# Optimization experiments

Hardware: AMD Instinct MI355X
Metric: run time of the kernel (lower is better)

## Reference

```python
import jax, jax.numpy as jnp
import numpy as np

B, N, C_IN = 32, 1024, 128
F0, F1, F2 = 64, 64, 64
OUT = 10
RATIOS = (0.8, 0.8)
EPS = 1e-5


def setup_inputs() -> dict:
    key = jax.random.key(0)
    ks = jax.random.split(key, 16)
    N_nodes = jax.random.randint(ks[0], (B,), N // 2, N + 1)
    mask = (jnp.arange(N)[None, :] < N_nodes[:, None]).astype(jnp.float32)
    x = jax.random.normal(ks[1], (B, N, C_IN), dtype=jnp.float32)
    # sparse-ish symmetric binary adjacency restricted to valid nodes
    A = (jax.random.uniform(ks[2], (B, N, N)) < 0.02).astype(jnp.float32)
    A = jnp.maximum(A, jnp.swapaxes(A, 1, 2))
    A = A * mask[:, :, None] * mask[:, None, :]
    def lin(k, fi, fo):
        b = 1.0 / np.sqrt(fi)
        kw, kb = jax.random.split(k)
        return (jax.random.uniform(kw, (fi, fo), minval=-b, maxval=b),
                jax.random.uniform(kb, (fo,), minval=-b, maxval=b))
    W0, b0 = lin(ks[3], C_IN, F0)
    W1, b1 = lin(ks[4], F0, F1)
    W2, b2 = lin(ks[5], F1, F2)
    bp0 = 1.0 / np.sqrt(F0)
    p0 = jax.random.uniform(ks[6], (F0, 1), minval=-bp0, maxval=bp0)
    bp1 = 1.0 / np.sqrt(F1)
    p1 = jax.random.uniform(ks[7], (F1, 1), minval=-bp1, maxval=bp1)
    Wfc, bfc = lin(ks[8], F2, OUT)
    return {"x": x, "A": A, "mask": mask, "N_nodes": N_nodes,
            "W0": W0, "b0": b0, "W1": W1, "b1": b1, "W2": W2, "b2": b2,
            "p0": p0, "p1": p1, "Wfc": Wfc, "bfc": bfc}


def _gconv(x, A, W, b):
    # Kipf-Welling normalized Laplacian conv, batched dense
    n = A.shape[1]
    A_hat = A + jnp.eye(n, dtype=A.dtype)[None]
    D = (jnp.sum(A_hat, axis=1) + EPS) ** -0.5  # [B,N]
    L = D[:, :, None] * A_hat * D[:, None, :]
    h = jnp.einsum('bnm,bmc->bnc', L, x) @ W + b
    return jax.nn.relu(h)


def _pool(x, A, mask, N_nodes, p, ratio):
    Bc, Nc, C = x.shape
    y = (x.reshape(Bc * Nc, C) @ p).reshape(Bc, Nc)
    y = y / jnp.sqrt(jnp.sum(p ** 2))
    N_remove = (N_nodes.astype(jnp.float32) * (1.0 - ratio)).astype(N_nodes.dtype)
    # remove the N_remove lowest-scoring valid nodes per graph
    y_eff = jnp.where(mask > 0, y, jnp.inf)
    ranks = jnp.argsort(jnp.argsort(y_eff, axis=1), axis=1)  # ascending rank
    new_mask = mask * (ranks >= N_remove[:, None]).astype(mask.dtype)
    x = x * jnp.tanh(y)[:, :, None] * new_mask[:, :, None]
    A = new_mask[:, :, None] * A * new_mask[:, None, :]
    return x, A, new_mask, N_nodes - N_remove


def reference(x, A, mask, N_nodes, W0, b0, W1, b1, W2, b2, p0, p1, Wfc, bfc):
    x = _gconv(x, A, W0, b0)
    x, A, mask, N_nodes = _pool(x, A, mask, N_nodes, p0, RATIOS[0])
    x = _gconv(x, A, W1, b1)
    x, A, mask, N_nodes = _pool(x, A, mask, N_nodes, p1, RATIOS[1])
    x = _gconv(x, A, W2, b2)
    x = jnp.max(x, axis=1)  # global max pool over nodes [B,F2]
    return x @ Wfc + bfc
```

## Files before the change

kernel.cpp:

```cpp
#include <hip/hip_runtime.h>
#include <cstdint>
#include <cstddef>

#define BB 32
#define NN 1024
#define CIN 128
#define FF 64
#define NOUT 10
#define CAP 128
#define EPSV 1e-5f

__global__ __launch_bounds__(256) void k_front(const float* __restrict__ A,
                                               const float* __restrict__ x,
                                               const float* __restrict__ W0,
                                               const int* __restrict__ Nn,
                                               const float* __restrict__ b2f,
                                               float* __restrict__ gmax,
                                               unsigned short* __restrict__ adj,
                                               int* __restrict__ cnt,
                                               float* __restrict__ c1,
                                               float* __restrict__ c2,
                                               float* __restrict__ T) {
    __shared__ __align__(16) float Wl[64 * 64];
    int tid = threadIdx.x;
    int wave = tid >> 6, lane = tid & 63;
    if (blockIdx.x >= 10240) {
        for (int i = tid; i < BB * 64; i += 256)
            gmax[i] = fmaxf(b2f[i & 63], 0.f);
        return;
    }
    if (blockIdx.x >= 8192) {
        int gid = blockIdx.x - 8192;
        int b = gid & 31;
        int cch = gid >> 5;
        if (cch * 16 >= Nn[b]) return;
        int row0 = (b << 10) + cch * 16;
        int rsub = lane >> 4, f0 = (lane & 15) * 4;
        int r = row0 + wave * 4 + rsub;
        const float4* xr = (const float4*)(x + (size_t)r * CIN);
        float4 acc = {0.f, 0.f, 0.f, 0.f};
#pragma unroll
        for (int kc = 0; kc < 2; ++kc) {
            if (kc) __syncthreads();
            for (int t = tid; t < 64 * 16; t += 256)
                ((float4*)Wl)[t] = ((const float4*)W0)[kc * 1024 + t];
            __syncthreads();
#pragma unroll 4
            for (int k4 = 0; k4 < 16; ++k4) {
                float4 xv = xr[kc * 16 + k4];
                float4 w0 = *(const float4*)&Wl[(k4 * 4 + 0) * 64 + f0];
                float4 w1 = *(const float4*)&Wl[(k4 * 4 + 1) * 64 + f0];
                float4 w2 = *(const float4*)&Wl[(k4 * 4 + 2) * 64 + f0];
                float4 w3 = *(const float4*)&Wl[(k4 * 4 + 3) * 64 + f0];
                acc.x += xv.x * w0.x; acc.y += xv.x * w0.y; acc.z += xv.x * w0.z; acc.w += xv.x * w0.w;
                acc.x += xv.y * w1.x; acc.y += xv.y * w1.y; acc.z += xv.y * w1.z; acc.w += xv.y * w1.w;
                acc.x += xv.z * w2.x; acc.y += xv.z * w2.y; acc.z += xv.z * w2.z; acc.w += xv.z * w2.w;
                acc.x += xv.w * w3.x; acc.y += xv.w * w3.y; acc.z += xv.w * w3.z; acc.w += xv.w * w3.w;
            }
        }
        *(float4*)&T[(size_t)r * 64 + f0] = acc;
    } else {
        int r = blockIdx.x * 4 + wave;
        int b = r >> 10;
        int Nb = Nn[b];
        int rl = r & 1023;
        if (rl >= Nb) {
            if (lane == 0) {
                cnt[r] = 0;
                float D = 1.0f / sqrtf(1.0f + EPSV);
                c1[r] = D;
                c2[r] = D * D;
            }
            return;
        }
        unsigned short* adjs = ((unsigned short*)Wl) + wave * CAP;
        const float4* Arow = (const float4*)(A + (size_t)r * NN);
        int nch = (Nb + 255) >> 8;
        float4 z4 = {0.f, 0.f, 0.f, 0.f};
        float4 v0 = Arow[lane];
        float4 v1 = Arow[64 + lane];
        float4 v2 = (nch > 2) ? Arow[128 + lane] : z4;
        float4 v3 = (nch > 3) ? Arow[192 + lane] : z4;
        int c = 0;
        unsigned long long lt = (lane == 0) ? 0ULL : ((1ULL << lane) - 1ULL);
        float4 vv[4] = {v0, v1, v2, v3};
#pragma unroll
        for (int it = 0; it < 4; ++it) {
            float4 v = vv[it];
            int j0 = it * 256 + lane * 4;
            unsigned long long m0 = __ballot(v.x != 0.f);
            unsigned long long m1 = __ballot(v.y != 0.f);
            unsigned long long m2 = __ballot(v.z != 0.f);
            unsigned long long m3 = __ballot(v.w != 0.f);
            int before = __popcll(m0 & lt) + __popcll(m1 & lt) +
                         __popcll(m2 & lt) + __popcll(m3 & lt);
            int p = c + before;
            if (v.x != 0.f) { if (p < CAP) adjs[p] = (unsigned short)(j0 + 0); ++p; }
            if (v.y != 0.f) { if (p < CAP) adjs[p] = (unsigned short)(j0 + 1); ++p; }
            if (v.z != 0.f) { if (p < CAP) adjs[p] = (unsigned short)(j0 + 2); ++p; }
            if (v.w != 0.f) { if (p < CAP) adjs[p] = (unsigned short)(j0 + 3); ++p; }
            c += __popcll(m0) + __popcll(m1) + __popcll(m2) + __popcll(m3);
        }
        int cc = (c > CAP) ? CAP : c;
        uint32_t* dst = (uint32_t*)(adj + (size_t)r * CAP);
        if (lane * 2 < cc) dst[lane] = ((const uint32_t*)adjs)[lane];
        if (lane == 0) {
            cnt[r] = cc;
            float D = 1.0f / sqrtf((float)c + 1.0f + EPSV);
            c1[r] = D;
            c2[r] = D * D;
        }
    }
}

__global__ __launch_bounds__(256) void k_mid(const unsigned short* __restrict__ adj,
                                             const int* __restrict__ cnt,
                                             const float* __restrict__ nm,
                                             float* __restrict__ c1, float* __restrict__ c2,
                                             const float* __restrict__ Xin,
                                             const float* __restrict__ W,
                                             const float* __restrict__ y,
                                             float* __restrict__ T,
                                             const int* __restrict__ Nn) {
    __shared__ __align__(16) float Wl[64 * 64];
    int tid = threadIdx.x;
    if (blockIdx.x >= 8192) {
        int gid = blockIdx.x - 8192;
        int b = gid & 31;
        int cch = gid >> 5;
        if (cch * 16 >= Nn[b]) return;
        int row0 = (b << 10) + cch * 16;
        for (int t = tid; t < 64 * 16; t += 256)
            ((float4*)Wl)[t] = ((const float4*)W)[t];
        __syncthreads();
        int wave = tid >> 6, lane = tid & 63;
        int rsub = lane >> 4, f0 = (lane & 15) * 4;
        int r = row0 + wave * 4 + rsub;
        float sc = tanhf(y[r]) * nm[r];
        const float4* xr = (const float4*)(Xin + (size_t)r * 64);
        float4 acc = {0.f, 0.f, 0.f, 0.f};
#pragma unroll 4
        for (int k4 = 0; k4 < 16; ++k4) {
            float4 xv = xr[k4];
            float4 w0 = *(const float4*)&Wl[(k4 * 4 + 0) * 64 + f0];
            float4 w1 = *(const float4*)&Wl[(k4 * 4 + 1) * 64 + f0];
            float4 w2 = *(const float4*)&Wl[(k4 * 4 + 2) * 64 + f0];
            float4 w3 = *(const float4*)&Wl[(k4 * 4 + 3) * 64 + f0];
            acc.x += xv.x * w0.x; acc.y += xv.x * w0.y; acc.z += xv.x * w0.z; acc.w += xv.x * w0.w;
            acc.x += xv.y * w1.x; acc.y += xv.y * w1.y; acc.z += xv.y * w1.z; acc.w += xv.y * w1.w;
            acc.x += xv.z * w2.x; acc.y += xv.z * w2.y; acc.z += xv.z * w2.z; acc.w += xv.z * w2.w;
            acc.x += xv.w * w3.x; acc.y += xv.w * w3.y; acc.z += xv.w * w3.z; acc.w += xv.w * w3.w;
        }
        acc.x *= sc; acc.y *= sc; acc.z *= sc; acc.w *= sc;
        *(float4*)&T[(size_t)r * 64 + f0] = acc;
    } else {
        int wave = tid >> 6, lane = tid & 63;
        int r = blockIdx.x * 4 + wave;
        int b = r >> 10;
        if ((r & 1023) >= Nn[b]) return;
        const unsigned short* arow = adj + (size_t)r * CAP;
        const float* nmb = nm + (b << 10);
        int n = cnt[r];
        float s = 0.f;
        if (lane < n)      s  = nmb[arow[lane]];
        if (lane + 64 < n) s += nmb[arow[lane + 64]];
        for (int sh = 32; sh; sh >>= 1) s += __shfl_xor(s, sh, 64);
        if (lane == 0) {
            float m = nm[r];
            float D = 1.0f / sqrtf(m * s + 1.0f + EPSV);
            c1[r] = m * D;
            c2[r] = D * D;
        }
    }
}

__global__ __launch_bounds__(256) void k_spmm(const unsigned short* __restrict__ adj,
                                              const int* __restrict__ cnt,
                                              const float* __restrict__ c1,
                                              const float* __restrict__ c2,
                                              const float* __restrict__ T,
                                              const float* __restrict__ bias,
                                              float* __restrict__ X,
                                              const float* __restrict__ p,
                                              float* __restrict__ y,
                                              float* __restrict__ gmax,
                                              const int* __restrict__ Nn) {
    __shared__ __align__(16) float c1s[NN];
    __shared__ float red[4][64];
    int b   = blockIdx.x & 31;
    int cch = blockIdx.x >> 5;
    int Nb = Nn[b];
    if (cch * 16 >= Nb) return;
    int tid = threadIdx.x;
    int n4 = (Nb + 3) >> 2;
    if (tid < n4) ((float4*)c1s)[tid] = ((const float4*)(c1 + (b << 10)))[tid];
    __syncthreads();
    int wave = tid >> 6, lane = tid & 63;
    int r0 = (b << 10) + cch * 16 + wave * 4;
    const float* Tb = T + ((size_t)(b << 10) << 6);
    float bv = bias[lane];
    float pv = 0.f, ppinv = 0.f;
    if (p != nullptr) {
        pv = p[lane];
        float pp = pv * pv;
        for (int s = 32; s; s >>= 1) pp += __shfl_xor(pp, s, 64);
        ppinv = 1.0f / sqrtf(pp);
    }
    float vmax = 0.f;
#pragma unroll
    for (int rr = 0; rr < 4; ++rr) {
        int r = r0 + rr;
        int rl = r & 1023;
        if (rl >= Nb) break;
        const unsigned short* arow = adj + (size_t)r * CAP;
        int n = cnt[r];
        float acc0 = 0.f, acc1 = 0.f, acc2 = 0.f, acc3 = 0.f;
        int t = 0;
        for (; t + 4 <= n; t += 4) {
            ushort4 j4 = *(const ushort4*)(arow + t);
            acc0 += c1s[j4.x] * Tb[((int)j4.x << 6) + lane];
            acc1 += c1s[j4.y] * Tb[((int)j4.y << 6) + lane];
            acc2 += c1s[j4.z] * Tb[((int)j4.z << 6) + lane];
            acc3 += c1s[j4.w] * Tb[((int)j4.w << 6) + lane];
        }
        for (; t < n; ++t) {
            int j = arow[t];
            acc0 += c1s[j] * Tb[(j << 6) + lane];
        }
        float acc = (acc0 + acc1) + (acc2 + acc3);
        float o = c1s[rl] * acc + c2[r] * T[((size_t)r << 6) + lane] + bv;
        o = fmaxf(o, 0.f);
        if (X != nullptr) X[((size_t)r << 6) + lane] = o;
        if (p != nullptr) {
            float a = o * pv;
            for (int s = 32; s; s >>= 1) a += __shfl_xor(a, s, 64);
            if (lane == 0) y[r] = a * ppinv;
        }
        vmax = fmaxf(vmax, o);
    }
    if (gmax != nullptr) {
        red[wave][lane] = vmax;
        __syncthreads();
        if (wave == 0) {
            float m = fmaxf(fmaxf(red[0][lane], red[1][lane]),
                            fmaxf(red[2][lane], red[3][lane]));
            atomicMax((int*)&gmax[(b << 6) + lane], __float_as_int(m));
        }
    }
}

__global__ __launch_bounds__(256) void k_rank(const float* __restrict__ y,
                                              const float* __restrict__ maskSrc,
                                              const int* __restrict__ nsrc,
                                              const int* __restrict__ nbound,
                                              float* __restrict__ nmOut,
                                              int* __restrict__ ncur) {
    __shared__ __align__(16) float yv[NN];
    int b = blockIdx.x >> 4;
    int sub = blockIdx.x & 15;
    int tid = threadIdx.x;
    const float INF = __builtin_inff();
    int Nb = nbound[b];
    {
        float4 v;
        if (tid * 4 < Nb) {
            v = ((const float4*)(y + (b << 10)))[tid];
            float4 m = ((const float4*)(maskSrc + (b << 10)))[tid];
            v.x = (m.x > 0.f) ? v.x : INF;
            v.y = (m.y > 0.f) ? v.y : INF;
            v.z = (m.z > 0.f) ? v.z : INF;
            v.w = (m.w > 0.f) ? v.w : INF;
        } else {
            v.x = INF; v.y = INF; v.z = INF; v.w = INF;
        }
        ((float4*)yv)[tid] = v;
    }
    int n = nsrc[b];
    const float RM = (float)(1.0 - 0.8);
    int nrem = (int)((float)n * RM);
    if (sub == 0 && tid == 0) ncur[b] = n - nrem;
    __syncthreads();
    int i = (sub << 6) + (tid >> 2);
    int q = tid & 3;
    float yi = yv[i];
    int rank = 0;
    if (yi < INF) {
        const float4* jbase = (const float4*)yv + (q << 6);
        int j0 = q << 8;
        int tend = (Nb - j0 + 3) >> 2;
        if (tend > 64) tend = 64;
#pragma unroll 8
        for (int t = 0; t < tend; ++t) {
            float4 a = jbase[t];
            int j = j0 + t * 4;
            rank += (a.x < yi || (a.x == yi && j     < i)) ? 1 : 0;
            rank += (a.y < yi || (a.y == yi && j + 1 < i)) ? 1 : 0;
            rank += (a.z < yi || (a.z == yi && j + 2 < i)) ? 1 : 0;
            rank += (a.w < yi || (a.w == yi && j + 3 < i)) ? 1 : 0;
        }
    }
    rank += __shfl_xor(rank, 1, 64);
    rank += __shfl_xor(rank, 2, 64);
    if (q == 0) {
        float nmv = (yi < INF && rank >= nrem) ? 1.f : 0.f;
        nmOut[(b << 10) + i] = nmv;
    }
}

__global__ __launch_bounds__(64) void k_fc(const float* __restrict__ gmax,
                                           const float* __restrict__ Wfc,
                                           const float* __restrict__ bfc,
                                           float* __restrict__ out) {
    __shared__ float gl[64];
    int b = blockIdx.x, lane = threadIdx.x;
    gl[lane] = gmax[(b << 6) + lane];
    __syncthreads();
    if (lane < NOUT) {
        float acc = bfc[lane];
        for (int k = 0; k < 64; ++k) acc += gl[k] * Wfc[k * NOUT + lane];
        out[b * NOUT + lane] = acc;
    }
}

extern "C" void kernel_launch(void* const* d_in, const int* in_sizes, int n_in,
                              void* d_out, int out_size, void* d_ws, size_t ws_size,
                              hipStream_t stream) {
    const float* x    = (const float*)d_in[0];
    const float* A    = (const float*)d_in[1];
    const float* mask = (const float*)d_in[2];
    const int*   Nn   = (const int*)d_in[3];
    const float* W0   = (const float*)d_in[4];
    const float* b0   = (const float*)d_in[5];
    const float* W1   = (const float*)d_in[6];
    const float* b1   = (const float*)d_in[7];
    const float* W2   = (const float*)d_in[8];
    const float* b2   = (const float*)d_in[9];
    const float* p0   = (const float*)d_in[10];
    const float* p1   = (const float*)d_in[11];
    const float* Wfc  = (const float*)d_in[12];
    const float* bfc  = (const float*)d_in[13];
    float* out = (float*)d_out;

    char* ws = (char*)d_ws;
    size_t off = 0;
    auto alloc = [&](size_t bytes) -> void* {
        void* p = ws + off;
        off = (off + bytes + 255) & ~(size_t)255;
        return p;
    };
    unsigned short* adj = (unsigned short*)alloc((size_t)BB * NN * CAP * 2);
    int*   cnt  = (int*)  alloc((size_t)BB * NN * 4);
    float* X    = (float*)alloc((size_t)BB * NN * 64 * 4);
    float* T    = (float*)alloc((size_t)BB * NN * 64 * 4);
    float* c1   = (float*)alloc((size_t)BB * NN * 4);
    float* c2   = (float*)alloc((size_t)BB * NN * 4);
    float* y    = (float*)alloc((size_t)BB * NN * 4);
    float* nm0  = (float*)alloc((size_t)BB * NN * 4);
    float* nm1  = (float*)alloc((size_t)BB * NN * 4);
    int*   nc0  = (int*)  alloc((size_t)BB * 4);
    int*   nc1  = (int*)  alloc((size_t)BB * 4);
    float* gmax = (float*)alloc((size_t)BB * 64 * 4);

    k_front<<<8192 + 2048 + 1, 256, 0, stream>>>(A, x, W0, Nn, b2, gmax,
                                                 adj, cnt, c1, c2, T);
    k_spmm<<<2048, 256, 0, stream>>>(adj, cnt, c1, c2, T, b0, X, p0, y, nullptr, Nn);
    k_rank<<<BB * 16, 256, 0, stream>>>(y, mask, Nn, Nn, nm0, nc0);
    k_mid<<<8192 + 2048, 256, 0, stream>>>(adj, cnt, nm0, c1, c2, X, W1, y, T, Nn);
    k_spmm<<<2048, 256, 0, stream>>>(adj, cnt, c1, c2, T, b1, X, p1, y, nullptr, Nn);
    k_rank<<<BB * 16, 256, 0, stream>>>(y, nm0, nc0, Nn, nm1, nc1);
    k_mid<<<8192 + 2048, 256, 0, stream>>>(adj, cnt, nm1, c1, c2, X, W2, y, T, Nn);
    k_spmm<<<2048, 256, 0, stream>>>(adj, cnt, c1, c2, T, b2, nullptr, nullptr, nullptr,
                                     gmax, Nn);
    k_fc<<<BB, 64, 0, stream>>>(gmax, Wfc, bfc, out);
}
```

Measured before the change: 362.8 us.

## Fuse next-layer weight matmul into SpMM and merge rank with degree recompute

Each SpMM now multiplies its ReLU output row by the next layer's weight matrix using wave shuffles, and writes the transformed features directly. The tanh-score and mask scaling is applied on the fly from per-node shared arrays. The separate mid kernel goes away, and ranking plus masked-degree normalisation are fused into one kernel per graph. Ranking now uses packed 64-bit key comparisons. This cuts two launches and a round trip of the intermediate features. In exchange, the rank kernel runs on only 32 blocks, and the per-row matvec reads the weights from global memory per lane.

```diff
diff --git a/kernel.cpp b/kernel.cpp
--- a/kernel.cpp
+++ b/kernel.cpp
@@ -113,80 +113,18 @@
     }
 }
 
-__global__ __launch_bounds__(256) void k_mid(const unsigned short* __restrict__ adj,
-                                             const int* __restrict__ cnt,
-                                             const float* __restrict__ nm,
-                                             float* __restrict__ c1, float* __restrict__ c2,
-                                             const float* __restrict__ Xin,
-                                             const float* __restrict__ W,
-                                             const float* __restrict__ y,
-                                             float* __restrict__ T,
-                                             const int* __restrict__ Nn) {
-    __shared__ __align__(16) float Wl[64 * 64];
-    int tid = threadIdx.x;
-    if (blockIdx.x >= 8192) {
-        int gid = blockIdx.x - 8192;
-        int b = gid & 31;
-        int cch = gid >> 5;
-        if (cch * 16 >= Nn[b]) return;
-        int row0 = (b << 10) + cch * 16;
-        for (int t = tid; t < 64 * 16; t += 256)
-            ((float4*)Wl)[t] = ((const float4*)W)[t];
-        __syncthreads();
-        int wave = tid >> 6, lane = tid & 63;
-        int rsub = lane >> 4, f0 = (lane & 15) * 4;
-        int r = row0 + wave * 4 + rsub;
-        float sc = tanhf(y[r]) * nm[r];
-        const float4* xr = (const float4*)(Xin + (size_t)r * 64);
-        float4 acc = {0.f, 0.f, 0.f, 0.f};
-#pragma unroll 4
-        for (int k4 = 0; k4 < 16; ++k4) {
-            float4 xv = xr[k4];
-            float4 w0 = *(const float4*)&Wl[(k4 * 4 + 0) * 64 + f0];
-            float4 w1 = *(const float4*)&Wl[(k4 * 4 + 1) * 64 + f0];
-            float4 w2 = *(const float4*)&Wl[(k4 * 4 + 2) * 64 + f0];
-            float4 w3 = *(const float4*)&Wl[(k4 * 4 + 3) * 64 + f0];
-            acc.x += xv.x * w0.x; acc.y += xv.x * w0.y; acc.z += xv.x * w0.z; acc.w += xv.x * w0.w;
-            acc.x += xv.y * w1.x; acc.y += xv.y * w1.y; acc.z += xv.y * w1.z; acc.w += xv.y * w1.w;
-            acc.x += xv.z * w2.x; acc.y += xv.z * w2.y; acc.z += xv.z * w2.z; acc.w += xv.z * w2.w;
-            acc.x += xv.w * w3.x; acc.y += xv.w * w3.y; acc.z += xv.w * w3.z; acc.w += xv.w * w3.w;
-        }
-        acc.x *= sc; acc.y *= sc; acc.z *= sc; acc.w *= sc;
-        *(float4*)&T[(size_t)r * 64 + f0] = acc;
-    } else {
-        int wave = tid >> 6, lane = tid & 63;
-        int r = blockIdx.x * 4 + wave;
-        int b = r >> 10;
-        if ((r & 1023) >= Nn[b]) return;
-        const unsigned short* arow = adj + (size_t)r * CAP;
-        const float* nmb = nm + (b << 10);
-        int n = cnt[r];
-        float s = 0.f;
-        if (lane < n)      s  = nmb[arow[lane]];
-        if (lane + 64 < n) s += nmb[arow[lane + 64]];
-        for (int sh = 32; sh; sh >>= 1) s += __shfl_xor(s, sh, 64);
-        if (lane == 0) {
-            float m = nm[r];
-            float D = 1.0f / sqrtf(m * s + 1.0f + EPSV);
-            c1[r] = m * D;
-            c2[r] = D * D;
-        }
-    }
-}
-
-__global__ __launch_bounds__(256) void k_spmm(const unsigned short* __restrict__ adj,
-                                              const int* __restrict__ cnt,
-                                              const float* __restrict__ c1,
-                                              const float* __restrict__ c2,
-                                              const float* __restrict__ T,
-                                              const float* __restrict__ bias,
-                                              float* __restrict__ X,
-                                              const float* __restrict__ p,
-                                              float* __restrict__ y,
-                                              float* __restrict__ gmax,
-                                              const int* __restrict__ Nn) {
+__global__ __launch_bounds__(256) void k_spmm1(const unsigned short* __restrict__ adj,
+                                               const int* __restrict__ cnt,
+                                               const float* __restrict__ c1,
+                                               const float* __restrict__ c2,
+                                               const float* __restrict__ T,
+                                               const float* __restrict__ bias,
+                                               const float* __restrict__ p,
+                                               float* __restrict__ y,
+                                               const float* __restrict__ Wn,
+                                               float* __restrict__ Tout,
+                                               const int* __restrict__ Nn) {
     __shared__ __align__(16) float c1s[NN];
-    __shared__ float red[4][64];
     int b   = blockIdx.x & 31;
     int cch = blockIdx.x >> 5;
     int Nb = Nn[b];
@@ -199,14 +137,10 @@
     int r0 = (b << 10) + cch * 16 + wave * 4;
     const float* Tb = T + ((size_t)(b << 10) << 6);
     float bv = bias[lane];
-    float pv = 0.f, ppinv = 0.f;
-    if (p != nullptr) {
-        pv = p[lane];
-        float pp = pv * pv;
-        for (int s = 32; s; s >>= 1) pp += __shfl_xor(pp, s, 64);
-        ppinv = 1.0f / sqrtf(pp);
-    }
-    float vmax = 0.f;
+    float pv = p[lane];
+    float pp = pv * pv;
+    for (int s = 32; s; s >>= 1) pp += __shfl_xor(pp, s, 64);
+    float ppinv = 1.0f / sqrtf(pp);
 #pragma unroll
     for (int rr = 0; rr < 4; ++rr) {
         int r = r0 + rr;
@@ -230,37 +164,38 @@
         float acc = (acc0 + acc1) + (acc2 + acc3);
         float o = c1s[rl] * acc + c2[r] * T[((size_t)r << 6) + lane] + bv;
         o = fmaxf(o, 0.f);
-        if (X != nullptr) X[((size_t)r << 6) + lane] = o;
-        if (p != nullptr) {
+        {
             float a = o * pv;
             for (int s = 32; s; s >>= 1) a += __shfl_xor(a, s, 64);
             if (lane == 0) y[r] = a * ppinv;
         }
-        vmax = fmaxf(vmax, o);
-    }
-    if (gmax != nullptr) {
-        red[wave][lane] = vmax;
-        __syncthreads();
-        if (wave == 0) {
-            float m = fmaxf(fmaxf(red[0][lane], red[1][lane]),
-                            fmaxf(red[2][lane], red[3][lane]));
-            atomicMax((int*)&gmax[(b << 6) + lane], __float_as_int(m));
-        }
-    }
-}
-
-__global__ __launch_bounds__(256) void k_rank(const float* __restrict__ y,
-                                              const float* __restrict__ maskSrc,
-                                              const int* __restrict__ nsrc,
-                                              const int* __restrict__ nbound,
-                                              float* __restrict__ nmOut,
-                                              int* __restrict__ ncur) {
+        {
+            float tac = 0.f;
+#pragma unroll 16
+            for (int k = 0; k < 64; ++k)
+                tac = fmaf(__shfl(o, k, 64), Wn[(k << 6) + lane], tac);
+            Tout[((size_t)r << 6) + lane] = tac;
+        }
+    }
+}
+
+__global__ __launch_bounds__(256) void k_rankdeg(const float* __restrict__ y,
+                                                 const float* __restrict__ maskSrc,
+                                                 const int* __restrict__ nsrc,
+                                                 const int* __restrict__ Nn,
+                                                 const unsigned short* __restrict__ adj,
+                                                 const int* __restrict__ cnt,
+                                                 float* __restrict__ nmOut,
+                                                 int* __restrict__ ncur,
+                                                 float* __restrict__ csrcO,
+                                                 float* __restrict__ scsO) {
     __shared__ __align__(16) float yv[NN];
-    int b = blockIdx.x >> 4;
-    int sub = blockIdx.x & 15;
+    __shared__ __align__(16) unsigned long long kv[NN];
+    __shared__ float nml[NN];
+    int b = blockIdx.x;
     int tid = threadIdx.x;
     const float INF = __builtin_inff();
-    int Nb = nbound[b];
+    int Nb = Nn[b];
     {
         float4 v;
         if (tid * 4 < Nb) {
@@ -278,32 +213,144 @@
     int n = nsrc[b];
     const float RM = (float)(1.0 - 0.8);
     int nrem = (int)((float)n * RM);
-    if (sub == 0 && tid == 0) ncur[b] = n - nrem;
-    __syncthreads();
-    int i = (sub << 6) + (tid >> 2);
-    int q = tid & 3;
-    float yi = yv[i];
-    int rank = 0;
-    if (yi < INF) {
-        const float4* jbase = (const float4*)yv + (q << 6);
-        int j0 = q << 8;
-        int tend = (Nb - j0 + 3) >> 2;
-        if (tend > 64) tend = 64;
-#pragma unroll 8
-        for (int t = 0; t < tend; ++t) {
-            float4 a = jbase[t];
-            int j = j0 + t * 4;
-            rank += (a.x < yi || (a.x == yi && j     < i)) ? 1 : 0;
-            rank += (a.y < yi || (a.y == yi && j + 1 < i)) ? 1 : 0;
-            rank += (a.z < yi || (a.z == yi && j + 2 < i)) ? 1 : 0;
-            rank += (a.w < yi || (a.w == yi && j + 3 < i)) ? 1 : 0;
-        }
-    }
-    rank += __shfl_xor(rank, 1, 64);
-    rank += __shfl_xor(rank, 2, 64);
-    if (q == 0) {
-        float nmv = (yi < INF && rank >= nrem) ? 1.f : 0.f;
+    if (tid == 0) ncur[b] = n - nrem;
+    __syncthreads();
+#pragma unroll
+    for (int t = 0; t < 4; ++t) {
+        int i = tid + (t << 8);
+        unsigned int u = __float_as_uint(yv[i]);
+        u ^= (unsigned int)((int)u >> 31) | 0x80000000u;
+        kv[i] = ((unsigned long long)u << 10) | (unsigned int)i;
+    }
+    __syncthreads();
+    unsigned long long k0 = kv[tid], k1 = kv[tid + 256],
+                       k2 = kv[tid + 512], k3 = kv[tid + 768];
+    int r0 = 0, r1 = 0, r2 = 0, r3 = 0;
+    int nkc = (Nb + 1) >> 1;
+#pragma unroll 4
+    for (int c = 0; c < nkc; ++c) {
+        ulonglong2 a = ((const ulonglong2*)kv)[c];
+        r0 += (a.x < k0) + (a.y < k0);
+        r1 += (a.x < k1) + (a.y < k1);
+        r2 += (a.x < k2) + (a.y < k2);
+        r3 += (a.x < k3) + (a.y < k3);
+    }
+    int rk[4] = {r0, r1, r2, r3};
+#pragma unroll
+    for (int t = 0; t < 4; ++t) {
+        int i = tid + (t << 8);
+        float nmv = (yv[i] < INF && rk[t] >= nrem) ? 1.f : 0.f;
+        nml[i] = nmv;
         nmOut[(b << 10) + i] = nmv;
+    }
+    __syncthreads();
+#pragma unroll
+    for (int t = 0; t < 4; ++t) {
+        int i = tid + (t << 8);
+        if (i < Nb) {
+            int gr = (b << 10) + i;
+            float m = nml[i];
+            int nn = cnt[gr];
+            const unsigned short* ar = adj + (size_t)gr * CAP;
+            float s = 0.f;
+            int tt = 0;
+            for (; tt + 4 <= nn; tt += 4) {
+                ushort4 j4 = *(const ushort4*)(ar + tt);
+                s += nml[j4.x] + nml[j4.y] + nml[j4.z] + nml[j4.w];
+            }
+            for (; tt < nn; ++tt) s += nml[ar[tt]];
+            float D = 1.0f / sqrtf(m * s + 1.0f + EPSV);
+            csrcO[gr] = m * D;
+            scsO[gr] = tanhf(yv[i]) * m;
+        }
+    }
+}
+
+__global__ __launch_bounds__(256) void k_spmm23(const unsigned short* __restrict__ adj,
+                                                const int* __restrict__ cnt,
+                                                const float* __restrict__ csrc,
+                                                const float* __restrict__ scs,
+                                                const float* __restrict__ Tin,
+                                                const float* __restrict__ bias,
+                                                const float* __restrict__ p,
+                                                float* __restrict__ y,
+                                                const float* __restrict__ Wn,
+                                                float* __restrict__ Tout,
+                                                float* __restrict__ gmax,
+                                                const int* __restrict__ Nn) {
+    __shared__ __align__(16) float csrcs[NN];
+    __shared__ __align__(16) float scss[NN];
+    __shared__ float red[4][64];
+    int b   = blockIdx.x & 31;
+    int cch = blockIdx.x >> 5;
+    int Nb = Nn[b];
+    if (cch * 16 >= Nb) return;
+    int tid = threadIdx.x;
+    int n4 = (Nb + 3) >> 2;
+    if (tid < n4) {
+        ((float4*)csrcs)[tid] = ((const float4*)(csrc + (b << 10)))[tid];
+        ((float4*)scss)[tid]  = ((const float4*)(scs  + (b << 10)))[tid];
+    }
+    __syncthreads();
+    int wave = tid >> 6, lane = tid & 63;
+    int r0 = (b << 10) + cch * 16 + wave * 4;
+    const float* Tb = Tin + ((size_t)(b << 10) << 6);
+    float bv = bias[lane];
+    float pv = 0.f, ppinv = 0.f;
+    if (p != nullptr) {
+        pv = p[lane];
+        float pp = pv * pv;
+        for (int s = 32; s; s >>= 1) pp += __shfl_xor(pp, s, 64);
+        ppinv = 1.0f / sqrtf(pp);
+    }
+    float vmax = 0.f;
+#pragma unroll
+    for (int rr = 0; rr < 4; ++rr) {
+        int r = r0 + rr;
+        int rl = r & 1023;
+        if (rl >= Nb) break;
+        const unsigned short* arow = adj + (size_t)r * CAP;
+        int n = cnt[r];
+        float acc0 = 0.f, acc1 = 0.f, acc2 = 0.f, acc3 = 0.f;
+        int t = 0;
+        for (; t + 4 <= n; t += 4) {
+            ushort4 j4 = *(const ushort4*)(arow + t);
+            acc0 += csrcs[j4.x] * (scss[j4.x] * Tb[((int)j4.x << 6) + lane]);
+            acc1 += csrcs[j4.y] * (scss[j4.y] * Tb[((int)j4.y << 6) + lane]);
+            acc2 += csrcs[j4.z] * (scss[j4.z] * Tb[((int)j4.z << 6) + lane]);
+            acc3 += csrcs[j4.w] * (scss[j4.w] * Tb[((int)j4.w << 6) + lane]);
+        }
+        for (; t < n; ++t) {
+            int j = arow[t];
+            acc0 += csrcs[j] * (scss[j] * Tb[(j << 6) + lane]);
+        }
+        float acc = (acc0 + acc1) + (acc2 + acc3);
+        float cd = csrcs[rl];
+        float selfv = scss[rl] * Tin[((size_t)r << 6) + lane];
+        float o = cd * acc + (cd * cd) * selfv + bv;
+        o = fmaxf(o, 0.f);
+        if (p != nullptr) {
+            float a = o * pv;
+            for (int s = 32; s; s >>= 1) a += __shfl_xor(a, s, 64);
+            if (lane == 0) y[r] = a * ppinv;
+        }
+        if (Wn != nullptr) {
+            float tac = 0.f;
+#pragma unroll 16
+            for (int k = 0; k < 64; ++k)
+                tac = fmaf(__shfl(o, k, 64), Wn[(k << 6) + lane], tac);
+            Tout[((size_t)r << 6) + lane] = tac;
+        }
+        vmax = fmaxf(vmax, o);
+    }
+    if (gmax != nullptr) {
+        red[wave][lane] = vmax;
+        __syncthreads();
+        if (wave == 0) {
+            float m = fmaxf(fmaxf(red[0][lane], red[1][lane]),
+                            fmaxf(red[2][lane], red[3][lane]));
+            atomicMax((int*)&gmax[(b << 6) + lane], __float_as_int(m));
+        }
     }
 }
 
@@ -363,13 +410,12 @@
 
     k_front<<<8192 + 2048 + 1, 256, 0, stream>>>(A, x, W0, Nn, b2, gmax,
                                                  adj, cnt, c1, c2, T);
-    k_spmm<<<2048, 256, 0, stream>>>(adj, cnt, c1, c2, T, b0, X, p0, y, nullptr, Nn);
-    k_rank<<<BB * 16, 256, 0, stream>>>(y, mask, Nn, Nn, nm0, nc0);
-    k_mid<<<8192 + 2048, 256, 0, stream>>>(adj, cnt, nm0, c1, c2, X, W1, y, T, Nn);
-    k_spmm<<<2048, 256, 0, stream>>>(adj, cnt, c1, c2, T, b1, X, p1, y, nullptr, Nn);
-    k_rank<<<BB * 16, 256, 0, stream>>>(y, nm0, nc0, Nn, nm1, nc1);
-    k_mid<<<8192 + 2048, 256, 0, stream>>>(adj, cnt, nm1, c1, c2, X, W2, y, T, Nn);
-    k_spmm<<<2048, 256, 0, stream>>>(adj, cnt, c1, c2, T, b2, nullptr, nullptr, nullptr,
-                                     gmax, Nn);
+    k_spmm1<<<2048, 256, 0, stream>>>(adj, cnt, c1, c2, T, b0, p0, y, W1, X, Nn);
+    k_rankdeg<<<BB, 256, 0, stream>>>(y, mask, Nn, Nn, adj, cnt, nm0, nc0, c1, c2);
+    k_spmm23<<<2048, 256, 0, stream>>>(adj, cnt, c1, c2, X, b1, p1, y, W2, T,
+                                       nullptr, Nn);
+    k_rankdeg<<<BB, 256, 0, stream>>>(y, nm0, nc0, Nn, adj, cnt, nm1, nc1, c1, c2);
+    k_spmm23<<<2048, 256, 0, stream>>>(adj, cnt, c1, c2, T, b2, nullptr, nullptr,
+                                       nullptr, nullptr, gmax, Nn);
     k_fc<<<BB, 64, 0, stream>>>(gmax, Wfc, bfc, out);
 }
```

Measured after the change: 409.4 us. 1.13x slower.
